# Optimization experiments

Measured on AMD Instinct MI355X. Metric: run time of the kernel, lower is better.

The kernel has to match this reference:

```python
import jax, jax.numpy as jnp
import numpy as np

B, IN, OUT = 512, 4096, 11008


def setup_inputs() -> dict:
    key = jax.random.key(0)
    k_x, k_stored, k_sign, k_scale, k_bias = jax.random.split(key, 5)
    x = jax.random.normal(k_x, (B, IN), dtype=jnp.float32)
    # QINS encoding: stored uint8 magnitude in [1, 255], sign in {-1, +1}
    stored = jax.random.randint(k_stored, (OUT, IN), 1, 256, dtype=jnp.int32)
    sign = 2 * jax.random.randint(k_sign, (OUT, IN), 0, 2, dtype=jnp.int32) - 1
    # log-range from from_linear's fallback calibration: weights in [e^-10, e^0]
    log_min = jnp.asarray(-10.0, dtype=jnp.float32)
    log_max = jnp.asarray(0.0, dtype=jnp.float32)
    # per-channel calibration scale, clamped to [0.5, 2.0] in from_linear
    scale = jax.random.uniform(k_scale, (OUT,), dtype=jnp.float32, minval=0.5, maxval=2.0)
    bias = jax.random.normal(k_bias, (OUT,), dtype=jnp.float32) * 0.01
    return {"x": x, "stored": stored, "sign": sign, "log_min": log_min,
            "log_max": log_max, "scale": scale, "bias": bias}


def reference(x, stored, sign, log_min, log_max, scale, bias):
    # Reconstruct fp32 weight from log-scale uint8 encoding (QINS)
    normalized = (255.0 - stored.astype(jnp.float32)) / 254.0      # [OUT, IN]
    log_w = log_min + normalized * (log_max - log_min)
    weight = sign.astype(jnp.float32) * jnp.exp(log_w)             # [OUT, IN]
    # y = (x @ W^T + b) * scale   (per-output-channel scale)
    out = jnp.einsum('bi,oi->bo', x, weight) + bias
    return out * scale
```

## Files before the change

kernel.cpp:

```cpp
#include <hip/hip_runtime.h>
#include <hip/hip_bf16.h>

#define B_DIM   512
#define IN_DIM  4096
#define OUT_DIM 11008
#define PB      (B_DIM * OUT_DIM)

typedef __bf16 bf16x4 __attribute__((ext_vector_type(4)));
typedef __bf16 bf16x8 __attribute__((ext_vector_type(8)));
typedef float  floatx4 __attribute__((ext_vector_type(4)));

__global__ __launch_bounds__(256) void conv_x_kernel(
    const float* __restrict__ x, __bf16* __restrict__ xb) {
  int idx = blockIdx.x * blockDim.x + threadIdx.x;
  float4 v = ((const float4*)x)[idx];
  bf16x4 o;
  o[0] = (__bf16)v.x; o[1] = (__bf16)v.y; o[2] = (__bf16)v.z; o[3] = (__bf16)v.w;
  ((bf16x4*)xb)[idx] = o;
}

__device__ __forceinline__ void gl_lds16(const void* g, void* l) {
  __builtin_amdgcn_global_load_lds(
      (const __attribute__((address_space(1))) void*)g,
      (__attribute__((address_space(3))) void*)l, 16, 0, 0);
}

__device__ __forceinline__ float dec1f(int s, int g, float lmin, float slope) {
  float e = __expf(fmaf((float)(255 - s), slope, lmin));
  return __uint_as_float(__float_as_uint(e) ^ ((unsigned)g & 0x80000000u));
}

__device__ __forceinline__ bf16x8 dec8(int4 sl, int4 sh, int4 gl, int4 gh,
                                       float lmin, float slope) {
  bf16x8 w;
  w[0] = (__bf16)dec1f(sl.x, gl.x, lmin, slope);
  w[1] = (__bf16)dec1f(sl.y, gl.y, lmin, slope);
  w[2] = (__bf16)dec1f(sl.z, gl.z, lmin, slope);
  w[3] = (__bf16)dec1f(sl.w, gl.w, lmin, slope);
  w[4] = (__bf16)dec1f(sh.x, gh.x, lmin, slope);
  w[5] = (__bf16)dec1f(sh.y, gh.y, lmin, slope);
  w[6] = (__bf16)dec1f(sh.z, gh.z, lmin, slope);
  w[7] = (__bf16)dec1f(sh.w, gh.w, lmin, slope);
  return w;
}

__global__ __launch_bounds__(256, 3) void fused_qins_gemm_kernel(
    const __bf16* __restrict__ A,
    const int* __restrict__ stored,
    const int* __restrict__ sign,
    const float* __restrict__ logmin, const float* __restrict__ logmax,
    float* __restrict__ part) {
  constexpr int K = IN_DIM, N = OUT_DIM;
  constexpr int BK = 32;
  constexpr int NT = 2048 / BK;

  __shared__ __align__(16) __bf16 sA[2][128 * BK];
  __shared__ __align__(16) __bf16 sB[2][128 * BK];

  const int tid  = threadIdx.x;
  const int lane = tid & 63;
  const int wave = tid >> 6;
  const int wm   = (wave >> 1) * 64;
  const int wn   = (wave & 1) * 64;
  const int m16  = lane & 15;
  const int q    = lane >> 4;

  const int wg  = blockIdx.x;
  const int g   = (wg & 7) * 86 + (wg >> 3);
  const int kh  = g / 344;
  const int rem = g % 344;
  const int bm0 = (rem & 3) * 128;
  const int bn0 = (rem >> 2) * 128;
  const int kbase = kh * 2048;

  const float lmin  = logmin[0];
  const float slope = (logmax[0] - lmin) * (1.0f / 254.0f);

  const int arow = tid >> 2;
  const int achk = (tid & 3) ^ (arow & 3);
  const __bf16* gA0 = A + (size_t)(bm0 + arow) * K + kbase + achk * 8;
  const __bf16* gA1 = gA0 + (size_t)64 * K;

  const int rB  = tid >> 1;
  const int bq2 = (tid & 1) * 2;
  const int* pS = stored + (size_t)(bn0 + rB) * K + kbase + bq2 * 8;
  const int* pG = sign   + (size_t)(bn0 + rB) * K + kbase + bq2 * 8;
  const int wOff0 = rB * BK + ((bq2       ^ (rB & 3)) * 8);
  const int wOff1 = rB * BK + (((bq2 + 1) ^ (rB & 3)) * 8);

  const int slotB = (q ^ (m16 & 3)) * 8;

  floatx4 acc[4][4] = {};

  int4 s0, s1, s2, s3, g0, g1, g2, g3;
  s0 = *(const int4*)(pS);     s1 = *(const int4*)(pS + 4);
  s2 = *(const int4*)(pS + 8); s3 = *(const int4*)(pS + 12);
  g0 = *(const int4*)(pG);     g1 = *(const int4*)(pG + 4);
  g2 = *(const int4*)(pG + 8); g3 = *(const int4*)(pG + 12);
  *(bf16x8*)&sB[0][wOff0] = dec8(s0, s1, g0, g1, lmin, slope);
  *(bf16x8*)&sB[0][wOff1] = dec8(s2, s3, g2, g3, lmin, slope);
  gl_lds16(gA0, &sA[0][tid * 8]);
  gl_lds16(gA1, &sA[0][2048 + tid * 8]);
  s0 = *(const int4*)(pS + BK);     s1 = *(const int4*)(pS + BK + 4);
  s2 = *(const int4*)(pS + BK + 8); s3 = *(const int4*)(pS + BK + 12);
  g0 = *(const int4*)(pG + BK);     g1 = *(const int4*)(pG + BK + 4);
  g2 = *(const int4*)(pG + BK + 8); g3 = *(const int4*)(pG + BK + 12);
  __syncthreads();

  for (int t = 0; t < NT; ++t) {
    const int c = t & 1;

    *(bf16x8*)&sB[c ^ 1][wOff0] = dec8(s0, s1, g0, g1, lmin, slope);
    *(bf16x8*)&sB[c ^ 1][wOff1] = dec8(s2, s3, g2, g3, lmin, slope);

    const int ktA = ((t + 1 < NT) ? (t + 1) : 0) * BK;
    gl_lds16(gA0 + ktA, &sA[c ^ 1][tid * 8]);
    gl_lds16(gA1 + ktA, &sA[c ^ 1][2048 + tid * 8]);

    const int ktB = ((t + 2 < NT) ? (t + 2) : 0) * BK;
    s0 = *(const int4*)(pS + ktB);     s1 = *(const int4*)(pS + ktB + 4);
    s2 = *(const int4*)(pS + ktB + 8); s3 = *(const int4*)(pS + ktB + 12);
    g0 = *(const int4*)(pG + ktB);     g1 = *(const int4*)(pG + ktB + 4);
    g2 = *(const int4*)(pG + ktB + 8); g3 = *(const int4*)(pG + ktB + 12);

    bf16x8 afr[4], bfr[4];
#pragma unroll
    for (int mi = 0; mi < 4; ++mi)
      afr[mi] = *(const bf16x8*)&sA[c][(wm + mi * 16 + m16) * BK + slotB];
#pragma unroll
    for (int ni = 0; ni < 4; ++ni)
      bfr[ni] = *(const bf16x8*)&sB[c][(wn + ni * 16 + m16) * BK + slotB];

#pragma unroll
    for (int mi = 0; mi < 4; ++mi)
#pragma unroll
      for (int ni = 0; ni < 4; ++ni)
        acc[mi][ni] = __builtin_amdgcn_mfma_f32_16x16x32_bf16(
            afr[mi], bfr[ni], acc[mi][ni], 0, 0, 0);

    __syncthreads();
  }

  float* p = part + (size_t)kh * PB;
#pragma unroll
  for (int ni = 0; ni < 4; ++ni) {
    const int col = bn0 + wn + ni * 16 + m16;
#pragma unroll
    for (int mi = 0; mi < 4; ++mi) {
#pragma unroll
      for (int r = 0; r < 4; ++r) {
        const int row = bm0 + wm + mi * 16 + q * 4 + r;
        p[(size_t)row * N + col] = acc[mi][ni][r];
      }
    }
  }
}

__global__ __launch_bounds__(256) void reduce_kernel(
    const float* __restrict__ part, const float* __restrict__ scale,
    const float* __restrict__ bias, float* __restrict__ out) {
  const int i4  = blockIdx.x * blockDim.x + threadIdx.x;
  const int col = (i4 % (OUT_DIM / 4)) * 4;
  float4 a = ((const float4*)part)[i4];
  float4 b = ((const float4*)(part + PB))[i4];
  float4 sc = *(const float4*)(scale + col);
  float4 bb = *(const float4*)(bias + col);
  float4 o;
  o.x = (a.x + b.x + bb.x) * sc.x;
  o.y = (a.y + b.y + bb.y) * sc.y;
  o.z = (a.z + b.z + bb.z) * sc.z;
  o.w = (a.w + b.w + bb.w) * sc.w;
  ((float4*)out)[i4] = o;
}

extern "C" void kernel_launch(void* const* d_in, const int* in_sizes, int n_in,
                              void* d_out, int out_size, void* d_ws, size_t ws_size,
                              hipStream_t stream) {
  const float* x      = (const float*)d_in[0];
  const int*   stored = (const int*)d_in[1];
  const int*   sign   = (const int*)d_in[2];
  const float* logmin = (const float*)d_in[3];
  const float* logmax = (const float*)d_in[4];
  const float* scale  = (const float*)d_in[5];
  const float* bias   = (const float*)d_in[6];
  float* out = (float*)d_out;

  float*  wsP = (float*)d_ws;
  __bf16* wsX = (__bf16*)(wsP + 2 * (size_t)PB);

  conv_x_kernel<<<2048, 256, 0, stream>>>(x, wsX);
  fused_qins_gemm_kernel<<<688, 256, 0, stream>>>(
      wsX, stored, sign, logmin, logmax, wsP);
  reduce_kernel<<<PB / 4 / 256, 256, 0, stream>>>(wsP, scale, bias, out);
}
```

Baseline: 479.5 us.

## Halve N tile to 64 and raise occupancy to five waves per SIMD

The GEMM tile shrinks from 128x128 to 128x64 output columns, so each thread decodes half as many weights per k-step and holds a 4x2 accumulator instead of 4x4. This doubles the grid to 1376 blocks and raises the launch-bounds occupancy hint from 3 to 5, with a remapped block-to-tile swizzle. The goal is more latency hiding for the exp-heavy decode and the global loads. The cost is that each A tile is reused across fewer columns, so x traffic doubles and there are fewer MFMAs per LDS read.

```diff
diff --git a/kernel.cpp b/kernel.cpp
--- a/kernel.cpp
+++ b/kernel.cpp
@@ -44,7 +44,7 @@
   return w;
 }
 
-__global__ __launch_bounds__(256, 3) void fused_qins_gemm_kernel(
+__global__ __launch_bounds__(256, 5) void fused_qins_gemm_kernel(
     const __bf16* __restrict__ A,
     const int* __restrict__ stored,
     const int* __restrict__ sign,
@@ -55,22 +55,21 @@
   constexpr int NT = 2048 / BK;
 
   __shared__ __align__(16) __bf16 sA[2][128 * BK];
-  __shared__ __align__(16) __bf16 sB[2][128 * BK];
+  __shared__ __align__(16) __bf16 sB[2][64 * BK];
 
   const int tid  = threadIdx.x;
   const int lane = tid & 63;
   const int wave = tid >> 6;
   const int wm   = (wave >> 1) * 64;
-  const int wn   = (wave & 1) * 64;
+  const int wn   = (wave & 1) * 32;
   const int m16  = lane & 15;
   const int q    = lane >> 4;
 
   const int wg  = blockIdx.x;
-  const int g   = (wg & 7) * 86 + (wg >> 3);
-  const int kh  = g / 344;
-  const int rem = g % 344;
-  const int bm0 = (rem & 3) * 128;
-  const int bn0 = (rem >> 2) * 128;
+  const int g   = (wg & 7) * 172 + (wg >> 3);
+  const int bn0 = (g >> 3) * 64;
+  const int kh  = (g >> 2) & 1;
+  const int bm0 = (g & 3) * 128;
   const int kbase = kh * 2048;
 
   const float lmin  = logmin[0];
@@ -81,60 +80,51 @@
   const __bf16* gA0 = A + (size_t)(bm0 + arow) * K + kbase + achk * 8;
   const __bf16* gA1 = gA0 + (size_t)64 * K;
 
-  const int rB  = tid >> 1;
-  const int bq2 = (tid & 1) * 2;
-  const int* pS = stored + (size_t)(bn0 + rB) * K + kbase + bq2 * 8;
-  const int* pG = sign   + (size_t)(bn0 + rB) * K + kbase + bq2 * 8;
-  const int wOff0 = rB * BK + ((bq2       ^ (rB & 3)) * 8);
-  const int wOff1 = rB * BK + (((bq2 + 1) ^ (rB & 3)) * 8);
+  const int rB = tid >> 2;
+  const int cB = tid & 3;
+  const int* pS = stored + (size_t)(bn0 + rB) * K + kbase + cB * 8;
+  const int* pG = sign   + (size_t)(bn0 + rB) * K + kbase + cB * 8;
+  const int wOff = rB * BK + ((cB ^ (rB & 3)) * 8);
 
-  const int slotB = (q ^ (m16 & 3)) * 8;
+  const int slotR = (q ^ (m16 & 3)) * 8;
 
-  floatx4 acc[4][4] = {};
+  floatx4 acc[4][2] = {};
 
-  int4 s0, s1, s2, s3, g0, g1, g2, g3;
-  s0 = *(const int4*)(pS);     s1 = *(const int4*)(pS + 4);
-  s2 = *(const int4*)(pS + 8); s3 = *(const int4*)(pS + 12);
-  g0 = *(const int4*)(pG);     g1 = *(const int4*)(pG + 4);
-  g2 = *(const int4*)(pG + 8); g3 = *(const int4*)(pG + 12);
-  *(bf16x8*)&sB[0][wOff0] = dec8(s0, s1, g0, g1, lmin, slope);
-  *(bf16x8*)&sB[0][wOff1] = dec8(s2, s3, g2, g3, lmin, slope);
+  int4 s0, s1, g0, g1;
+  s0 = *(const int4*)(pS); s1 = *(const int4*)(pS + 4);
+  g0 = *(const int4*)(pG); g1 = *(const int4*)(pG + 4);
+  *(bf16x8*)&sB[0][wOff] = dec8(s0, s1, g0, g1, lmin, slope);
   gl_lds16(gA0, &sA[0][tid * 8]);
   gl_lds16(gA1, &sA[0][2048 + tid * 8]);
-  s0 = *(const int4*)(pS + BK);     s1 = *(const int4*)(pS + BK + 4);
-  s2 = *(const int4*)(pS + BK + 8); s3 = *(const int4*)(pS + BK + 12);
-  g0 = *(const int4*)(pG + BK);     g1 = *(const int4*)(pG + BK + 4);
-  g2 = *(const int4*)(pG + BK + 8); g3 = *(const int4*)(pG + BK + 12);
+  s0 = *(const int4*)(pS + BK); s1 = *(const int4*)(pS + BK + 4);
+  g0 = *(const int4*)(pG + BK); g1 = *(const int4*)(pG + BK + 4);
   __syncthreads();
 
   for (int t = 0; t < NT; ++t) {
     const int c = t & 1;
 
-    *(bf16x8*)&sB[c ^ 1][wOff0] = dec8(s0, s1, g0, g1, lmin, slope);
-    *(bf16x8*)&sB[c ^ 1][wOff1] = dec8(s2, s3, g2, g3, lmin, slope);
+    *(bf16x8*)&sB[c ^ 1][wOff] = dec8(s0, s1, g0, g1, lmin, slope);
+
+    const int ktB = ((t + 2 < NT) ? (t + 2) : 0) * BK;
+    s0 = *(const int4*)(pS + ktB); s1 = *(const int4*)(pS + ktB + 4);
+    g0 = *(const int4*)(pG + ktB); g1 = *(const int4*)(pG + ktB + 4);
 
     const int ktA = ((t + 1 < NT) ? (t + 1) : 0) * BK;
     gl_lds16(gA0 + ktA, &sA[c ^ 1][tid * 8]);
     gl_lds16(gA1 + ktA, &sA[c ^ 1][2048 + tid * 8]);
 
-    const int ktB = ((t + 2 < NT) ? (t + 2) : 0) * BK;
-    s0 = *(const int4*)(pS + ktB);     s1 = *(const int4*)(pS + ktB + 4);
-    s2 = *(const int4*)(pS + ktB + 8); s3 = *(const int4*)(pS + ktB + 12);
-    g0 = *(const int4*)(pG + ktB);     g1 = *(const int4*)(pG + ktB + 4);
-    g2 = *(const int4*)(pG + ktB + 8); g3 = *(const int4*)(pG + ktB + 12);
-
-    bf16x8 afr[4], bfr[4];
+    bf16x8 afr[4], bfr[2];
 #pragma unroll
     for (int mi = 0; mi < 4; ++mi)
-      afr[mi] = *(const bf16x8*)&sA[c][(wm + mi * 16 + m16) * BK + slotB];
+      afr[mi] = *(const bf16x8*)&sA[c][(wm + mi * 16 + m16) * BK + slotR];
 #pragma unroll
-    for (int ni = 0; ni < 4; ++ni)
-      bfr[ni] = *(const bf16x8*)&sB[c][(wn + ni * 16 + m16) * BK + slotB];
+    for (int ni = 0; ni < 2; ++ni)
+      bfr[ni] = *(const bf16x8*)&sB[c][(wn + ni * 16 + m16) * BK + slotR];
 
 #pragma unroll
     for (int mi = 0; mi < 4; ++mi)
 #pragma unroll
-      for (int ni = 0; ni < 4; ++ni)
+      for (int ni = 0; ni < 2; ++ni)
         acc[mi][ni] = __builtin_amdgcn_mfma_f32_16x16x32_bf16(
             afr[mi], bfr[ni], acc[mi][ni], 0, 0, 0);
 
@@ -143,7 +133,7 @@
 
   float* p = part + (size_t)kh * PB;
 #pragma unroll
-  for (int ni = 0; ni < 4; ++ni) {
+  for (int ni = 0; ni < 2; ++ni) {
     const int col = bn0 + wn + ni * 16 + m16;
 #pragma unroll
     for (int mi = 0; mi < 4; ++mi) {
@@ -189,7 +179,7 @@
   __bf16* wsX = (__bf16*)(wsP + 2 * (size_t)PB);
 
   conv_x_kernel<<<2048, 256, 0, stream>>>(x, wsX);
-  fused_qins_gemm_kernel<<<688, 256, 0, stream>>>(
+  fused_qins_gemm_kernel<<<1376, 256, 0, stream>>>(
       wsX, stored, sign, logmin, logmax, wsP);
   reduce_kernel<<<PB / 4 / 256, 256, 0, stream>>>(wsP, scale, bias, out);
 }
```

After: 514.1 us. 7.2% more time.
